# Kernel tuning notes

Hardware: AMD Instinct MI355X
Metric: run time of the kernel (lower is better)

The kernel has to match this reference:

```python
import jax, jax.numpy as jnp
import numpy as np

LN_EPS = 1e-6          # flax nn.LayerNorm default
ATTN_EPS = 1e-9        # numerical_stabilizer default


def ln_points(x, scale, bias):
    """flax LayerNorm(reduction_axes=-2): stats over points axis, affine over feature axis."""
    mu = jnp.mean(x, axis=-2, keepdims=True)
    var = jnp.mean(jnp.square(x), axis=-2, keepdims=True) - jnp.square(mu)
    return (x - mu) * jax.lax.rsqrt(var + LN_EPS) * scale + bias


def self_attention_layer(x, wq_i, bq_i, wk_i, bk_i, wv_i, bv_i, wo_i, bo_i, ls_i, lb_i):
    # 1x1 convs == pointwise linears
    q = x @ wq_i + bq_i                                  # [B,N,C]
    k = x @ wk_i + bk_i
    v = x @ wv_i + bv_i
    attn = jnp.einsum('bmc,bnc->bmn', q, k)              # [B,M,N]
    attn = jax.nn.softmax(attn, axis=-1)
    # extra offset-attention renorm: divide by column sums (axis=1)
    attn = attn / (ATTN_EPS + jnp.sum(attn, axis=1, keepdims=True))
    # einsum '...MN,...NC->...NC' reduces M: scales v by column sums
    col = jnp.sum(attn, axis=1)                          # [B,N]
    out = col[..., None] * v                             # [B,N,C]
    out = out @ wo_i + bo_i
    out = jax.nn.relu(ln_points(out, ls_i, lb_i))
    return out + x


def setup_inputs() -> dict:
    key = jax.random.key(0)
    ks = jax.random.split(key, 16)
    B, N, IN, C, F, L = 2, 4096, 3, 256, 1024, 4
    s_in = 1.0 / np.sqrt(IN)
    s_c = 1.0 / np.sqrt(C)
    s_f = 1.0 / np.sqrt(L * C)
    return {
        'inputs': jax.random.normal(ks[0], (B, N, IN), jnp.float32),
        'w0': jax.random.normal(ks[1], (IN, C), jnp.float32) * s_in,
        'b0': jnp.zeros((C,), jnp.float32),
        'ln0_s': jnp.ones((C,), jnp.float32),
        'ln0_b': jnp.zeros((C,), jnp.float32),
        'w1': jax.random.normal(ks[2], (C, C), jnp.float32) * s_c,
        'b1': jnp.zeros((C,), jnp.float32),
        'ln1_s': jnp.ones((C,), jnp.float32),
        'ln1_b': jnp.zeros((C,), jnp.float32),
        'wq': jax.random.normal(ks[3], (L, C, C), jnp.float32) * s_c,
        'bq': jnp.zeros((L, C), jnp.float32),
        'wk': jax.random.normal(ks[4], (L, C, C), jnp.float32) * s_c,
        'bk': jnp.zeros((L, C), jnp.float32),
        'wv': jax.random.normal(ks[5], (L, C, C), jnp.float32) * s_c,
        'bv': jnp.zeros((L, C), jnp.float32),
        'wo': jax.random.normal(ks[6], (L, C, C), jnp.float32) * s_c,
        'bo': jnp.zeros((L, C), jnp.float32),
        'attn_ln_s': jnp.ones((L, C), jnp.float32),
        'attn_ln_b': jnp.zeros((L, C), jnp.float32),
        'wf': jax.random.normal(ks[7], (L * C, F), jnp.float32) * s_f,
        'bf': jnp.zeros((F,), jnp.float32),
    }


def reference(inputs, w0, b0, ln0_s, ln0_b, w1, b1, ln1_s, ln1_b,
              wq, bq, wk, bk, wv, bv, wo, bo, attn_ln_s, attn_ln_b, wf, bf):
    # pre-conv stack
    out = ln_points(inputs @ w0 + b0, ln0_s, ln0_b)
    out = ln_points(out @ w1 + b1, ln1_s, ln1_b)
    # attention stack (4 structurally identical layers, concatenated)
    attn_outs = []
    for i in range(wq.shape[0]):
        out = self_attention_layer(out, wq[i], bq[i], wk[i], bk[i],
                                   wv[i], bv[i], wo[i], bo[i],
                                   attn_ln_s[i], attn_ln_b[i])
        attn_outs.append(out)
    out = jnp.concatenate(attn_outs, axis=-1)            # [B,N,4C]
    out = out @ wf + bf                                  # [B,N,F]
    return out
```

## Files before the change

### kernel.cpp

```cpp
#include <hip/hip_runtime.h>

#define BB 2
#define NN 4096
#define CC 256
#define FF 1024
#define NLAYER 4
#define RR (BB*NN)
#define SPL 16
#define QKLD (3*CC)
#define NEG_BIG (-1e30f)
#define LOG2E 1.44269504f

typedef _Float16 h16;
typedef __attribute__((ext_vector_type(8))) _Float16 half8;
typedef __attribute__((ext_vector_type(4))) float f32x4;
typedef __attribute__((ext_vector_type(16))) float f32x16;

#define WAITVM(n) asm volatile("s_waitcnt vmcnt(" #n ")" ::: "memory")

__device__ __forceinline__ void gload16(const h16* g, h16* l) {
    __builtin_amdgcn_global_load_lds((const __attribute__((address_space(1))) void*)g,
                                     (__attribute__((address_space(3))) void*)l, 16, 0, 0);
}

template<int ROWS>
__device__ __forceinline__ void stage_rows(const h16* __restrict__ src, int ld,
    int row0, int c0, h16* lds, int tid)
{
    int w = tid >> 6;
    #pragma unroll
    for (int t = 0; t < ROWS/32; ++t) {
        int slot = t*256 + tid;
        int row = slot >> 3;
        int pp  = slot & 7;
        int piece = pp ^ (row & 7);
        gload16(src + (size_t)(row0 + row)*ld + c0 + piece*8,
                lds + (t*256 + w*64)*8);
    }
}

__device__ __forceinline__ half8 frag_ld(const h16* lds, int row, int pl) {
    return *(const half8*)(lds + row*64 + ((pl ^ (row & 7))*8));
}

__global__ __launch_bounds__(256) void pct_wtrans(const float* __restrict__ W,
    h16* __restrict__ WT, int K, int N, int dstride, float scale)
{
    __shared__ h16 t[32][33];
    const float* Wl = W + (size_t)blockIdx.z*K*N;
    h16* WTl = WT + (size_t)blockIdx.z*dstride;
    int k0 = blockIdx.x*32, n0 = blockIdx.y*32;
    int tx = threadIdx.x & 31, ty = threadIdx.x >> 5;
    #pragma unroll
    for (int i = ty; i < 32; i += 8)
        t[i][tx] = (h16)(Wl[(size_t)(k0+i)*N + n0 + tx] * scale);
    __syncthreads();
    #pragma unroll
    for (int i = ty; i < 32; i += 8)
        WTl[(size_t)(n0+i)*K + k0 + tx] = t[tx][i];
}

__global__ __launch_bounds__(256) void pct_wtrans_qkv(const float* __restrict__ wq,
    const float* __restrict__ wk, const float* __restrict__ wv, h16* __restrict__ WT)
{
    __shared__ h16 t[32][33];
    int z = blockIdx.z;
    int which = z >> 2, layer = z & 3;
    const float* Wl = (which == 0 ? wq : which == 1 ? wk : wv) + (size_t)layer*CC*CC;
    h16* WTl = WT + (size_t)layer*QKLD*CC + (size_t)which*CC*CC;
    float scale = (which == 0) ? LOG2E : 1.0f;
    int k0 = blockIdx.x*32, n0 = blockIdx.y*32;
    int tx = threadIdx.x & 31, ty = threadIdx.x >> 5;
    #pragma unroll
    for (int i = ty; i < 32; i += 8)
        t[i][tx] = (h16)(Wl[(size_t)(k0+i)*CC + n0 + tx] * scale);
    __syncthreads();
    #pragma unroll
    for (int i = ty; i < 32; i += 8)
        WTl[(size_t)(n0+i)*CC + k0 + tx] = t[tx][i];
}

__global__ __launch_bounds__(256) void pct_bias3(const float* __restrict__ bq,
    const float* __restrict__ bk, const float* __restrict__ bv, float* __restrict__ o)
{
    int l = blockIdx.x, c = threadIdx.x;
    o[l*QKLD + c]        = bq[l*CC + c] * LOG2E;
    o[l*QKLD + CC + c]   = bk[l*CC + c];
    o[l*QKLD + 2*CC + c] = bv[l*CC + c];
}

__global__ __launch_bounds__(256) void pct_embed(const float* __restrict__ inp,
    const float* __restrict__ w0, const float* __restrict__ b0,
    h16* __restrict__ out, float* __restrict__ sums)
{
    int c = threadIdx.x;
    int r0 = blockIdx.x * 64;
    float wa = w0[c], wb = w0[CC+c], wcv = w0[2*CC+c], bb = b0[c];
    float s1 = 0.f, s2 = 0.f;
    #pragma unroll 4
    for (int i = 0; i < 64; ++i) {
        int r = r0 + i;
        float y = bb + inp[r*3+0]*wa + inp[r*3+1]*wb + inp[r*3+2]*wcv;
        h16 hy = (h16)y;
        out[(size_t)r*CC + c] = hy;
        float yf = (float)hy;
        s1 += yf; s2 += yf*yf;
    }
    int b = r0 >> 12;
    atomicAdd(&sums[((size_t)b*CC + c)*2 + 0], s1);
    atomicAdd(&sums[((size_t)b*CC + c)*2 + 1], s2);
}

__global__ __launch_bounds__(256) void pct_lnapply(const h16* __restrict__ x, int ldx,
    const float* __restrict__ sums, const float* __restrict__ scale, const float* __restrict__ bias,
    const h16* __restrict__ res, int ldr, h16* __restrict__ out, int ldo,
    int do_relu)
{
    int r = blockIdx.x*8 + (threadIdx.x >> 5);
    int cg = (threadIdx.x & 31) * 8;
    int b = r / NN;
    half8 xv = *(const half8*)(x + (size_t)r*ldx + cg);
    half8 rv;
    if (res) rv = *(const half8*)(res + (size_t)r*ldr + cg);
    half8 ov;
    #pragma unroll
    for (int j = 0; j < 8; ++j) {
        int c = cg + j;
        float s1 = sums[(b*CC + c)*2], s2 = sums[(b*CC + c)*2 + 1];
        float mu  = s1 * (1.f/NN);
        float var = s2 * (1.f/NN) - mu*mu;
        float rstd = rsqrtf(var + 1e-6f);
        float y = ((float)xv[j] - mu) * rstd * scale[c] + bias[c];
        if (do_relu) y = fmaxf(y, 0.f);
        if (res) y += (float)rv[j];
        ov[j] = (h16)y;
    }
    *(half8*)(out + (size_t)r*ldo + cg) = ov;
}

template<int BN, bool OUT_F32, bool CSTAT>
__global__ __launch_bounds__(256) void pct_gemm_f16(
    const h16* __restrict__ A, int lda,
    const h16* __restrict__ WT, const float* __restrict__ bias,
    void* __restrict__ outp, int ldo, int K, const float* __restrict__ rowS,
    float* __restrict__ csums)
{
    constexpr int BJ = BN/2;
    constexpr int NF = BJ/16;
    __shared__ __align__(16) h16 Asm[128*64];
    __shared__ __align__(16) h16 Bsm[BN*64];
    const int tid = threadIdx.x;
    const int lane = tid & 63, w = tid >> 6;
    const int ln = lane & 15, lq = lane >> 4;
    const int wr = w >> 1, wc = w & 1;
    const int m0 = blockIdx.x*128, n0 = blockIdx.y*BN;
    f32x4 acc[4][NF];
    #pragma unroll
    for (int i = 0; i < 4; ++i)
        #pragma unroll
        for (int j = 0; j < NF; ++j) acc[i][j] = (f32x4){0.f,0.f,0.f,0.f};
    for (int k0 = 0; k0 < K; k0 += 64) {
        stage_rows<128>(A, lda, m0, k0, Asm, tid);
        stage_rows<BN>(WT, K, n0, k0, Bsm, tid);
        __syncthreads();
        #pragma unroll
        for (int kk = 0; kk < 2; ++kk) {
            half8 af[4], bfr[NF];
            #pragma unroll
            for (int i = 0; i < 4; ++i) af[i] = frag_ld(Asm, wr*64 + i*16 + ln, kk*4 + lq);
            #pragma unroll
            for (int j = 0; j < NF; ++j) bfr[j] = frag_ld(Bsm, wc*BJ + j*16 + ln, kk*4 + lq);
            #pragma unroll
            for (int i = 0; i < 4; ++i)
                #pragma unroll
                for (int j = 0; j < NF; ++j)
                    acc[i][j] = __builtin_amdgcn_mfma_f32_16x16x32_f16(af[i], bfr[j], acc[i][j], 0, 0, 0);
        }
        __syncthreads();
    }
    float cs1[NF], cs2[NF];
    #pragma unroll
    for (int j = 0; j < NF; ++j) {
        int col = n0 + wc*BJ + j*16 + ln;
        float bv = bias[col];
        float s1 = 0.f, s2 = 0.f;
        #pragma unroll
        for (int i = 0; i < 4; ++i) {
            #pragma unroll
            for (int r = 0; r < 4; ++r) {
                int row = m0 + wr*64 + i*16 + lq*4 + r;
                float sc = 1.f;
                if (rowS) { float s = rowS[row]; sc = s / (1e-9f + s); }
                float v = acc[i][j][r] * sc + bv;
                if (OUT_F32) ((float*)outp)[(size_t)row*ldo + col] = v;
                else ((h16*)outp)[(size_t)row*ldo + col] = (h16)v;
                if (CSTAT) { s1 += v; s2 += v*v; }
            }
        }
        cs1[j] = s1; cs2[j] = s2;
    }
    if constexpr (CSTAT) {
        __shared__ float cred[2][2][BJ][2];
        #pragma unroll
        for (int j = 0; j < NF; ++j) {
            float s1 = cs1[j], s2 = cs2[j];
            s1 += __shfl_down(s1, 16); s1 += __shfl_down(s1, 32);
            s2 += __shfl_down(s2, 16); s2 += __shfl_down(s2, 32);
            if (lane < 16) {
                cred[wr][wc][j*16 + lane][0] = s1;
                cred[wr][wc][j*16 + lane][1] = s2;
            }
        }
        __syncthreads();
        if (tid < 2*BN) {
            int c = tid >> 1, st = tid & 1;
            int wcc = c >> 5, ci = c & 31;
            float v = cred[0][wcc][ci][st] + cred[1][wcc][ci][st];
            int b = m0 >> 12;
            atomicAdd(&csums[((size_t)b*CC + n0 + c)*2 + st], v);
        }
    }
}

__global__ __launch_bounds__(256) void attn_rowstats(const h16* __restrict__ QKV,
    float2* __restrict__ part)
{
    __shared__ __align__(16) h16 Ks[2][128*64];
    const int b = blockIdx.x, mt = blockIdx.y, sp = blockIdx.z;
    const int tid = threadIdx.x;
    const int lane = tid & 63, w = tid >> 6;
    const int ln2 = lane & 31, h = lane >> 5;
    const h16* qb = QKV + (size_t)b*NN*QKLD;
    const h16* kb = qb + CC;
    const int m0 = mt*128;
    const h16* qrow = qb + (size_t)(m0 + w*32 + ln2)*QKLD + h*8;
    half8 qreg[16];
    #pragma unroll
    for (int i = 0; i < 16; ++i) qreg[i] = *(const half8*)(qrow + i*16);

    const int nbeg = sp*(NN/SPL);
    constexpr int NT = (NN/SPL)/128;
    constexpr int NCH = NT*4;
    float rm = NEG_BIG, rs = 0.f;

    stage_rows<128>(kb, QKLD, nbeg, 0, Ks[0], tid);
    int id = 0;
    #pragma unroll
    for (int t = 0; t < NT; ++t) {
        f32x16 acc[4];
        #pragma unroll
        for (int j = 0; j < 4; ++j) acc[j] = (f32x16)(0.f);
        #pragma unroll
        for (int c = 0; c < 4; ++c, ++id) {
            if (id + 1 < NCH) {
                stage_rows<128>(kb, QKLD, nbeg + ((id+1) >> 2)*128, ((id+1) & 3)*64,
                                Ks[(id+1) & 1], tid);
                WAITVM(4);
            } else {
                WAITVM(0);
            }
            __builtin_amdgcn_s_barrier();
            const h16* buf = Ks[id & 1];
            __builtin_amdgcn_s_setprio(1);
            #pragma unroll
            for (int kk = 0; kk < 4; ++kk) {
                half8 bq = qreg[c*4 + kk];
                #pragma unroll
                for (int j = 0; j < 4; ++j) {
                    half8 af = frag_ld(buf, j*32 + ln2, kk*2 + h);
                    acc[j] = __builtin_amdgcn_mfma_f32_32x32x16_f16(af, bq, acc[j], 0, 0, 0);
                }
            }
            __builtin_amdgcn_s_setprio(0);
            __builtin_amdgcn_s_barrier();
        }
        float tm = NEG_BIG;
        #pragma unroll
        for (int j = 0; j < 4; ++j)
            #pragma unroll
            for (int g = 0; g < 16; g += 2)
                tm = fmaxf(tm, fmaxf(acc[j][g], acc[j][g+1]));
        if (tm > rm) { rs *= exp2f(rm - tm); rm = tm; }
        float s = 0.f;
        #pragma unroll
        for (int j = 0; j < 4; ++j)
            #pragma unroll
            for (int g = 0; g < 16; ++g)
                s += exp2f(acc[j][g] - rm);
        rs += s;
    }
    float mo = __shfl_xor(rm, 32, 64);
    float so = __shfl_xor(rs, 32, 64);
    float mn = fmaxf(rm, mo);
    float sm = rs*exp2f(rm - mn) + so*exp2f(mo - mn);
    if (lane < 32) {
        int m = m0 + w*32 + ln2;
        part[((size_t)b*NN + m)*SPL + sp] = make_float2(mn, sm);
    }
}

__global__ __launch_bounds__(256) void attn_colsums(const h16* __restrict__ QKV,
    const float2* __restrict__ part, float* __restrict__ S)
{
    __shared__ __align__(16) h16 Qs[2][128*64];
    __shared__ float2 rst_s[256];
    const int b = blockIdx.x, nt = blockIdx.y, sp = blockIdx.z;
    const int tid = threadIdx.x;
    const int lane = tid & 63, w = tid >> 6;
    const int ln2 = lane & 31, h = lane >> 5;
    const h16* qb = QKV + (size_t)b*NN*QKLD;
    const h16* kb = qb + CC;
    const int n0 = nt*128;
    const int mbeg = sp*(NN/SPL);

    {
        const float2* pp = part + ((size_t)b*NN + mbeg + tid)*SPL;
        float m = NEG_BIG;
        #pragma unroll
        for (int s = 0; s < SPL; ++s) m = fmaxf(m, pp[s].x);
        float sum = 0.f;
        #pragma unroll
        for (int s = 0; s < SPL; ++s) sum += pp[s].y * exp2f(pp[s].x - m);
        rst_s[tid] = make_float2(m, 1.0f / sum);
    }
    __syncthreads();

    const h16* krow = kb + (size_t)(n0 + w*32 + ln2)*QKLD + h*8;
    half8 kreg[16];
    #pragma unroll
    for (int i = 0; i < 16; ++i) kreg[i] = *(const half8*)(krow + i*16);

    constexpr int NT = (NN/SPL)/128;
    constexpr int NCH = NT*4;
    float cs = 0.f;

    stage_rows<128>(qb, QKLD, mbeg, 0, Qs[0], tid);
    int id = 0;
    #pragma unroll
    for (int t = 0; t < NT; ++t) {
        f32x16 acc[4];
        #pragma unroll
        for (int j = 0; j < 4; ++j) acc[j] = (f32x16)(0.f);
        #pragma unroll
        for (int c = 0; c < 4; ++c, ++id) {
            if (id + 1 < NCH) {
                stage_rows<128>(qb, QKLD, mbeg + ((id+1) >> 2)*128, ((id+1) & 3)*64,
                                Qs[(id+1) & 1], tid);
                WAITVM(4);
            } else {
                WAITVM(0);
            }
            __builtin_amdgcn_s_barrier();
            const h16* buf = Qs[id & 1];
            __builtin_amdgcn_s_setprio(1);
            #pragma unroll
            for (int kk = 0; kk < 4; ++kk) {
                half8 bk = kreg[c*4 + kk];
                #pragma unroll
                for (int j = 0; j < 4; ++j) {
                    half8 af = frag_ld(buf, j*32 + ln2, kk*2 + h);
                    acc[j] = __builtin_amdgcn_mfma_f32_32x32x16_f16(af, bk, acc[j], 0, 0, 0);
                }
            }
            __builtin_amdgcn_s_setprio(0);
            __builtin_amdgcn_s_barrier();
        }
        int mt0 = t*128;
        #pragma unroll
        for (int j = 0; j < 4; ++j) {
            #pragma unroll
            for (int g = 0; g < 16; ++g) {
                int mloc = mt0 + j*32 + (g & 3) + 8*(g >> 2) + 4*h;
                float2 st = rst_s[mloc];
                cs += exp2f(acc[j][g] - st.x) * st.y;
            }
        }
    }
    cs += __shfl_xor(cs, 32, 64);
    if (lane < 32) {
        int n = n0 + w*32 + ln2;
        atomicAdd(&S[(size_t)b*NN + n], cs);
    }
}

extern "C" void kernel_launch(void* const* d_in, const int* in_sizes, int n_in,
                              void* d_out, int out_size, void* d_ws, size_t ws_size,
                              hipStream_t stream)
{
    const float* inp  = (const float*)d_in[0];
    const float* w0   = (const float*)d_in[1];
    const float* b0   = (const float*)d_in[2];
    const float* ln0s = (const float*)d_in[3];
    const float* ln0b = (const float*)d_in[4];
    const float* w1   = (const float*)d_in[5];
    const float* b1   = (const float*)d_in[6];
    const float* ln1s = (const float*)d_in[7];
    const float* ln1b = (const float*)d_in[8];
    const float* wq   = (const float*)d_in[9];
    const float* bq   = (const float*)d_in[10];
    const float* wk   = (const float*)d_in[11];
    const float* bk   = (const float*)d_in[12];
    const float* wv   = (const float*)d_in[13];
    const float* bv   = (const float*)d_in[14];
    const float* wo   = (const float*)d_in[15];
    const float* bo   = (const float*)d_in[16];
    const float* alns = (const float*)d_in[17];
    const float* alnb = (const float*)d_in[18];
    const float* wf   = (const float*)d_in[19];
    const float* bfb  = (const float*)d_in[20];
    float* out = (float*)d_out;

    char* p = (char*)d_ws;
    auto alloc = [&](size_t bytes) { char* r = p; p += (bytes + 255) & ~255ULL; return r; };
    h16* t0    = (h16*)alloc((size_t)RR*CC*2);
    h16* t1    = (h16*)alloc((size_t)RR*CC*2);
    h16* t2    = (h16*)alloc((size_t)RR*CC*2);
    h16* x1    = (h16*)alloc((size_t)RR*CC*2);
    h16* qkv   = (h16*)alloc((size_t)RR*QKLD*2);
    h16* oh    = (h16*)alloc((size_t)RR*CC*2);
    h16* xcat  = (h16*)alloc((size_t)RR*FF*2);
    h16* w1T   = (h16*)alloc((size_t)CC*CC*2);
    h16* wqkvT = (h16*)alloc((size_t)NLAYER*QKLD*CC*2);
    h16* woT   = (h16*)alloc((size_t)NLAYER*CC*CC*2);
    h16* wfT   = (h16*)alloc((size_t)FF*FF*2);
    float* bqkv  = (float*)alloc((size_t)NLAYER*QKLD*4);
    float2* part  = (float2*)alloc((size_t)RR*SPL*8);
    float* Ssum  = (float*)alloc((size_t)NLAYER*RR*4);
    float* lns   = (float*)alloc((size_t)6*BB*CC*2*4);

    dim3 blk(256);

    hipMemsetAsync(Ssum, 0, (size_t)((char*)(lns + 6*BB*CC*2) - (char*)Ssum), stream);

    pct_wtrans<<<dim3(CC/32, CC/32, 1), blk, 0, stream>>>(w1, w1T, CC, CC, CC*CC, 1.f);
    pct_wtrans_qkv<<<dim3(CC/32, CC/32, 3*NLAYER), blk, 0, stream>>>(wq, wk, wv, wqkvT);
    pct_wtrans<<<dim3(CC/32, CC/32, NLAYER), blk, 0, stream>>>(wo, woT, CC, CC, CC*CC, 1.f);
    pct_wtrans<<<dim3(FF/32, FF/32, 1), blk, 0, stream>>>(wf, wfT, FF, FF, FF*FF, 1.f);
    pct_bias3<<<NLAYER, blk, 0, stream>>>(bq, bk, bv, bqkv);

    pct_embed<<<RR/64, blk, 0, stream>>>(inp, w0, b0, t0, lns + 0*BB*CC*2);
    pct_lnapply<<<RR/8, blk, 0, stream>>>(t0, CC, lns + 0*BB*CC*2, ln0s, ln0b, nullptr, 0, t1, CC, 0);
    pct_gemm_f16<64,false,true><<<dim3(RR/128, CC/64), blk, 0, stream>>>(
        t1, CC, w1T, b1, t2, CC, CC, nullptr, lns + 1*BB*CC*2);
    pct_lnapply<<<RR/8, blk, 0, stream>>>(t2, CC, lns + 1*BB*CC*2, ln1s, ln1b, nullptr, 0, x1, CC, 0);

    const h16* xin = x1; int ldx = CC;
    for (int i = 0; i < NLAYER; ++i) {
        pct_gemm_f16<64,false,false><<<dim3(RR/128, QKLD/64), blk, 0, stream>>>(
            xin, ldx, wqkvT + (size_t)i*QKLD*CC, bqkv + i*QKLD, qkv, QKLD, CC, nullptr, nullptr);

        attn_rowstats<<<dim3(BB, NN/128, SPL), blk, 0, stream>>>(qkv, part);
        attn_colsums<<<dim3(BB, NN/128, SPL), blk, 0, stream>>>(qkv, part, Ssum + (size_t)i*RR);

        pct_gemm_f16<64,false,true><<<dim3(RR/128, CC/64), blk, 0, stream>>>(
            qkv + 2*CC, QKLD, woT + (size_t)i*CC*CC, bo + i*CC, oh, CC, CC,
            Ssum + (size_t)i*RR, lns + (2+i)*BB*CC*2);

        pct_lnapply<<<RR/8, blk, 0, stream>>>(oh, CC, lns + (2+i)*BB*CC*2, alns + i*CC, alnb + i*CC,
                                              xin, ldx, xcat + i*CC, FF, 1);
        xin = xcat + i*CC; ldx = FF;
    }

    pct_gemm_f16<128,true,false><<<dim3(RR/128, FF/128), blk, 0, stream>>>(
        xcat, FF, wfT, bfb, out, FF, FF, nullptr, nullptr);
}
```

Measured before the change: 497.6 us.

## Interleave K/Q prefetch with MFMA steps and remap attention grid per XCD

The two attention kernels now issue the next tile's global-to-LDS loads one piece per kk step, after that step's fragments are read, so the copy is spread across the compute. The old code issued the whole stage up front and waited on a partial vmcnt. The wait is now a full vmcnt(0) at the top of each chunk, and the MFMA priority bump is narrowed to each group of four MFMAs. The grids are flattened to 1D and block ids are remapped so each XCD's blocks share one batch and neighbouring row tiles, which aims to improve L2 reuse of K and Q. Prefetch time now has less slack, and the full wait could expose load latency.

```diff
diff --git a/kernel.cpp b/kernel.cpp
--- a/kernel.cpp
+++ b/kernel.cpp
@@ -37,6 +37,18 @@
         gload16(src + (size_t)(row0 + row)*ld + c0 + piece*8,
                 lds + (t*256 + w*64)*8);
     }
+}
+
+__device__ __forceinline__ void stage_piece(const h16* __restrict__ src, int ld,
+    int row0, int c0, h16* lds, int tid, int t)
+{
+    int w = tid >> 6;
+    int slot = t*256 + tid;
+    int row = slot >> 3;
+    int pp  = slot & 7;
+    int piece = pp ^ (row & 7);
+    gload16(src + (size_t)(row0 + row)*ld + c0 + piece*8,
+            lds + (t*256 + w*64)*8);
 }
 
 __device__ __forceinline__ half8 frag_ld(const h16* lds, int row, int pl) {
@@ -226,7 +238,11 @@
     float2* __restrict__ part)
 {
     __shared__ __align__(16) h16 Ks[2][128*64];
-    const int b = blockIdx.x, mt = blockIdx.y, sp = blockIdx.z;
+    const int lid = blockIdx.x;
+    const int xcd = lid & 7;
+    const int b   = xcd >> 2;
+    const int r   = (lid >> 3)*4 + (xcd & 3);
+    const int mt  = r >> 4, sp = r & 15;
     const int tid = threadIdx.x;
     const int lane = tid & 63, w = tid >> 6;
     const int ln2 = lane & 31, h = lane >> 5;
@@ -252,26 +268,25 @@
         for (int j = 0; j < 4; ++j) acc[j] = (f32x16)(0.f);
         #pragma unroll
         for (int c = 0; c < 4; ++c, ++id) {
-            if (id + 1 < NCH) {
-                stage_rows<128>(kb, QKLD, nbeg + ((id+1) >> 2)*128, ((id+1) & 3)*64,
-                                Ks[(id+1) & 1], tid);
-                WAITVM(4);
-            } else {
-                WAITVM(0);
-            }
+            WAITVM(0);
             __builtin_amdgcn_s_barrier();
             const h16* buf = Ks[id & 1];
-            __builtin_amdgcn_s_setprio(1);
+            const bool pf = (id + 1 < NCH);
+            const int prow = pf ? nbeg + ((id+1) >> 2)*128 : 0;
+            const int pcol = pf ? ((id+1) & 3)*64 : 0;
             #pragma unroll
             for (int kk = 0; kk < 4; ++kk) {
+                half8 af[4];
+                #pragma unroll
+                for (int j = 0; j < 4; ++j) af[j] = frag_ld(buf, j*32 + ln2, kk*2 + h);
+                if (pf) stage_piece(kb, QKLD, prow, pcol, Ks[(id+1) & 1], tid, kk);
                 half8 bq = qreg[c*4 + kk];
+                __builtin_amdgcn_s_setprio(1);
                 #pragma unroll
-                for (int j = 0; j < 4; ++j) {
-                    half8 af = frag_ld(buf, j*32 + ln2, kk*2 + h);
-                    acc[j] = __builtin_amdgcn_mfma_f32_32x32x16_f16(af, bq, acc[j], 0, 0, 0);
-                }
+                for (int j = 0; j < 4; ++j)
+                    acc[j] = __builtin_amdgcn_mfma_f32_32x32x16_f16(af[j], bq, acc[j], 0, 0, 0);
+                __builtin_amdgcn_s_setprio(0);
             }
-            __builtin_amdgcn_s_setprio(0);
             __builtin_amdgcn_s_barrier();
         }
         float tm = NEG_BIG;
@@ -304,7 +319,11 @@
 {
     __shared__ __align__(16) h16 Qs[2][128*64];
     __shared__ float2 rst_s[256];
-    const int b = blockIdx.x, nt = blockIdx.y, sp = blockIdx.z;
+    const int lid = blockIdx.x;
+    const int xcd = lid & 7;
+    const int b   = xcd >> 2;
+    const int r   = (lid >> 3)*4 + (xcd & 3);
+    const int nt  = r >> 4, sp = r & 15;
     const int tid = threadIdx.x;
     const int lane = tid & 63, w = tid >> 6;
     const int ln2 = lane & 31, h = lane >> 5;
@@ -343,26 +362,25 @@
         for (int j = 0; j < 4; ++j) acc[j] = (f32x16)(0.f);
         #pragma unroll
         for (int c = 0; c < 4; ++c, ++id) {
-            if (id + 1 < NCH) {
-                stage_rows<128>(qb, QKLD, mbeg + ((id+1) >> 2)*128, ((id+1) & 3)*64,
-                                Qs[(id+1) & 1], tid);
-                WAITVM(4);
-            } else {
-                WAITVM(0);
-            }
+            WAITVM(0);
             __builtin_amdgcn_s_barrier();
             const h16* buf = Qs[id & 1];
-            __builtin_amdgcn_s_setprio(1);
+            const bool pf = (id + 1 < NCH);
+            const int prow = pf ? mbeg + ((id+1) >> 2)*128 : 0;
+            const int pcol = pf ? ((id+1) & 3)*64 : 0;
             #pragma unroll
             for (int kk = 0; kk < 4; ++kk) {
+                half8 af[4];
+                #pragma unroll
+                for (int j = 0; j < 4; ++j) af[j] = frag_ld(buf, j*32 + ln2, kk*2 + h);
+                if (pf) stage_piece(qb, QKLD, prow, pcol, Qs[(id+1) & 1], tid, kk);
                 half8 bk = kreg[c*4 + kk];
+                __builtin_amdgcn_s_setprio(1);
                 #pragma unroll
-                for (int j = 0; j < 4; ++j) {
-                    half8 af = frag_ld(buf, j*32 + ln2, kk*2 + h);
-                    acc[j] = __builtin_amdgcn_mfma_f32_32x32x16_f16(af, bk, acc[j], 0, 0, 0);
-                }
+                for (int j = 0; j < 4; ++j)
+                    acc[j] = __builtin_amdgcn_mfma_f32_32x32x16_f16(af[j], bk, acc[j], 0, 0, 0);
+                __builtin_amdgcn_s_setprio(0);
             }
-            __builtin_amdgcn_s_setprio(0);
             __builtin_amdgcn_s_barrier();
         }
         int mt0 = t*128;
@@ -449,8 +467,8 @@
         pct_gemm_f16<64,false,false><<<dim3(RR/128, QKLD/64), blk, 0, stream>>>(
             xin, ldx, wqkvT + (size_t)i*QKLD*CC, bqkv + i*QKLD, qkv, QKLD, CC, nullptr, nullptr);
 
-        attn_rowstats<<<dim3(BB, NN/128, SPL), blk, 0, stream>>>(qkv, part);
-        attn_colsums<<<dim3(BB, NN/128, SPL), blk, 0, stream>>>(qkv, part, Ssum + (size_t)i*RR);
+        attn_rowstats<<<dim3(BB*(NN/128)*SPL), blk, 0, stream>>>(qkv, part);
+        attn_colsums<<<dim3(BB*(NN/128)*SPL), blk, 0, stream>>>(qkv, part, Ssum + (size_t)i*RR);
 
         pct_gemm_f16<64,false,true><<<dim3(RR/128, CC/64), blk, 0, stream>>>(
             qkv + 2*CC, QKLD, woT + (size_t)i*CC*CC, bo + i*CC, oh, CC, CC,
```

Result: slower. 518.5 us (+4.2%).

## Use 2x2 warp tiling in attention row-stat and column-sum kernels

Applied to the files above, without the earlier changes.

Changes the warp decomposition in attn_rowstats and attn_colsums from each warp owning 32 register rows against all 128 LDS rows to a 2x2 layout. Each warp now owns 64 register rows against 64 LDS rows, which halves the LDS fragment loads per MFMA and reuses each LDS fragment for two MFMAs. Row-stat partials double since each row now gets two partial max/sum pairs, so the partial buffer and the colsum merge loop grow accordingly. Register pressure rises (two sets of Q/K registers) and launch_bounds now requests 2 blocks per SIMD-group, which may cause spills.

```diff
diff --git a/kernel.cpp b/kernel.cpp
--- a/kernel.cpp
+++ b/kernel.cpp
@@ -222,7 +222,7 @@
     }
 }
 
-__global__ __launch_bounds__(256) void attn_rowstats(const h16* __restrict__ QKV,
+__global__ __launch_bounds__(256, 2) void attn_rowstats(const h16* __restrict__ QKV,
     float2* __restrict__ part)
 {
     __shared__ __align__(16) h16 Ks[2][128*64];
@@ -230,26 +230,32 @@
     const int tid = threadIdx.x;
     const int lane = tid & 63, w = tid >> 6;
     const int ln2 = lane & 31, h = lane >> 5;
+    const int wn = w & 1, wm = w >> 1;
     const h16* qb = QKV + (size_t)b*NN*QKLD;
     const h16* kb = qb + CC;
     const int m0 = mt*128;
-    const h16* qrow = qb + (size_t)(m0 + w*32 + ln2)*QKLD + h*8;
-    half8 qreg[16];
-    #pragma unroll
-    for (int i = 0; i < 16; ++i) qreg[i] = *(const half8*)(qrow + i*16);
+    half8 qreg[2][16];
+    #pragma unroll
+    for (int mh = 0; mh < 2; ++mh) {
+        const h16* qrow = qb + (size_t)(m0 + wm*64 + mh*32 + ln2)*QKLD + h*8;
+        #pragma unroll
+        for (int i = 0; i < 16; ++i) qreg[mh][i] = *(const half8*)(qrow + i*16);
+    }
 
     const int nbeg = sp*(NN/SPL);
     constexpr int NT = (NN/SPL)/128;
     constexpr int NCH = NT*4;
-    float rm = NEG_BIG, rs = 0.f;
+    float rm[2] = {NEG_BIG, NEG_BIG}, rs[2] = {0.f, 0.f};
 
     stage_rows<128>(kb, QKLD, nbeg, 0, Ks[0], tid);
     int id = 0;
     #pragma unroll
     for (int t = 0; t < NT; ++t) {
-        f32x16 acc[4];
-        #pragma unroll
-        for (int j = 0; j < 4; ++j) acc[j] = (f32x16)(0.f);
+        f32x16 acc[2][2];
+        #pragma unroll
+        for (int j = 0; j < 2; ++j)
+            #pragma unroll
+            for (int mh = 0; mh < 2; ++mh) acc[j][mh] = (f32x16)(0.f);
         #pragma unroll
         for (int c = 0; c < 4; ++c, ++id) {
             if (id + 1 < NCH) {
@@ -264,42 +270,52 @@
             __builtin_amdgcn_s_setprio(1);
             #pragma unroll
             for (int kk = 0; kk < 4; ++kk) {
-                half8 bq = qreg[c*4 + kk];
-                #pragma unroll
-                for (int j = 0; j < 4; ++j) {
-                    half8 af = frag_ld(buf, j*32 + ln2, kk*2 + h);
-                    acc[j] = __builtin_amdgcn_mfma_f32_32x32x16_f16(af, bq, acc[j], 0, 0, 0);
-                }
+                half8 af[2];
+                #pragma unroll
+                for (int j = 0; j < 2; ++j)
+                    af[j] = frag_ld(buf, wn*64 + j*32 + ln2, kk*2 + h);
+                #pragma unroll
+                for (int j = 0; j < 2; ++j)
+                    #pragma unroll
+                    for (int mh = 0; mh < 2; ++mh)
+                        acc[j][mh] = __builtin_amdgcn_mfma_f32_32x32x16_f16(
+                            af[j], qreg[mh][c*4 + kk], acc[j][mh], 0, 0, 0);
             }
             __builtin_amdgcn_s_setprio(0);
             __builtin_amdgcn_s_barrier();
         }
-        float tm = NEG_BIG;
-        #pragma unroll
-        for (int j = 0; j < 4; ++j)
-            #pragma unroll
-            for (int g = 0; g < 16; g += 2)
-                tm = fmaxf(tm, fmaxf(acc[j][g], acc[j][g+1]));
-        if (tm > rm) { rs *= exp2f(rm - tm); rm = tm; }
-        float s = 0.f;
-        #pragma unroll
-        for (int j = 0; j < 4; ++j)
-            #pragma unroll
-            for (int g = 0; g < 16; ++g)
-                s += exp2f(acc[j][g] - rm);
-        rs += s;
-    }
-    float mo = __shfl_xor(rm, 32, 64);
-    float so = __shfl_xor(rs, 32, 64);
-    float mn = fmaxf(rm, mo);
-    float sm = rs*exp2f(rm - mn) + so*exp2f(mo - mn);
-    if (lane < 32) {
-        int m = m0 + w*32 + ln2;
-        part[((size_t)b*NN + m)*SPL + sp] = make_float2(mn, sm);
-    }
-}
-
-__global__ __launch_bounds__(256) void attn_colsums(const h16* __restrict__ QKV,
+        #pragma unroll
+        for (int mh = 0; mh < 2; ++mh) {
+            float tm = NEG_BIG;
+            #pragma unroll
+            for (int j = 0; j < 2; ++j)
+                #pragma unroll
+                for (int g = 0; g < 16; g += 2)
+                    tm = fmaxf(tm, fmaxf(acc[j][mh][g], acc[j][mh][g+1]));
+            if (tm > rm[mh]) { rs[mh] *= exp2f(rm[mh] - tm); rm[mh] = tm; }
+            float s = 0.f;
+            #pragma unroll
+            for (int j = 0; j < 2; ++j)
+                #pragma unroll
+                for (int g = 0; g < 16; ++g)
+                    s += exp2f(acc[j][mh][g] - rm[mh]);
+            rs[mh] += s;
+        }
+    }
+    #pragma unroll
+    for (int mh = 0; mh < 2; ++mh) {
+        float mo = __shfl_xor(rm[mh], 32, 64);
+        float so = __shfl_xor(rs[mh], 32, 64);
+        float mn = fmaxf(rm[mh], mo);
+        float sm = rs[mh]*exp2f(rm[mh] - mn) + so*exp2f(mo - mn);
+        if (lane < 32) {
+            int m = m0 + wm*64 + mh*32 + ln2;
+            part[(((size_t)b*NN + m)*SPL + sp)*2 + wn] = make_float2(mn, sm);
+        }
+    }
+}
+
+__global__ __launch_bounds__(256, 2) void attn_colsums(const h16* __restrict__ QKV,
     const float2* __restrict__ part, float* __restrict__ S)
 {
     __shared__ __align__(16) h16 Qs[2][128*64];
@@ -308,39 +324,45 @@
     const int tid = threadIdx.x;
     const int lane = tid & 63, w = tid >> 6;
     const int ln2 = lane & 31, h = lane >> 5;
+    const int ws = w & 1, wn2 = w >> 1;
     const h16* qb = QKV + (size_t)b*NN*QKLD;
     const h16* kb = qb + CC;
     const int n0 = nt*128;
     const int mbeg = sp*(NN/SPL);
 
     {
-        const float2* pp = part + ((size_t)b*NN + mbeg + tid)*SPL;
+        const float2* pp = part + ((size_t)b*NN + mbeg + tid)*SPL*2;
         float m = NEG_BIG;
         #pragma unroll
-        for (int s = 0; s < SPL; ++s) m = fmaxf(m, pp[s].x);
+        for (int s = 0; s < SPL*2; ++s) m = fmaxf(m, pp[s].x);
         float sum = 0.f;
         #pragma unroll
-        for (int s = 0; s < SPL; ++s) sum += pp[s].y * exp2f(pp[s].x - m);
+        for (int s = 0; s < SPL*2; ++s) sum += pp[s].y * exp2f(pp[s].x - m);
         rst_s[tid] = make_float2(m, 1.0f / sum);
     }
     __syncthreads();
 
-    const h16* krow = kb + (size_t)(n0 + w*32 + ln2)*QKLD + h*8;
-    half8 kreg[16];
-    #pragma unroll
-    for (int i = 0; i < 16; ++i) kreg[i] = *(const half8*)(krow + i*16);
+    half8 kreg[2][16];
+    #pragma unroll
+    for (int nh = 0; nh < 2; ++nh) {
+        const h16* krow = kb + (size_t)(n0 + wn2*64 + nh*32 + ln2)*QKLD + h*8;
+        #pragma unroll
+        for (int i = 0; i < 16; ++i) kreg[nh][i] = *(const half8*)(krow + i*16);
+    }
 
     constexpr int NT = (NN/SPL)/128;
     constexpr int NCH = NT*4;
-    float cs = 0.f;
+    float cs[2] = {0.f, 0.f};
 
     stage_rows<128>(qb, QKLD, mbeg, 0, Qs[0], tid);
     int id = 0;
     #pragma unroll
     for (int t = 0; t < NT; ++t) {
-        f32x16 acc[4];
-        #pragma unroll
-        for (int j = 0; j < 4; ++j) acc[j] = (f32x16)(0.f);
+        f32x16 acc[2][2];
+        #pragma unroll
+        for (int js = 0; js < 2; ++js)
+            #pragma unroll
+            for (int nh = 0; nh < 2; ++nh) acc[js][nh] = (f32x16)(0.f);
         #pragma unroll
         for (int c = 0; c < 4; ++c, ++id) {
             if (id + 1 < NCH) {
@@ -355,31 +377,41 @@
             __builtin_amdgcn_s_setprio(1);
             #pragma unroll
             for (int kk = 0; kk < 4; ++kk) {
-                half8 bk = kreg[c*4 + kk];
-                #pragma unroll
-                for (int j = 0; j < 4; ++j) {
-                    half8 af = frag_ld(buf, j*32 + ln2, kk*2 + h);
-                    acc[j] = __builtin_amdgcn_mfma_f32_32x32x16_f16(af, bk, acc[j], 0, 0, 0);
-                }
+                half8 af[2];
+                #pragma unroll
+                for (int js = 0; js < 2; ++js)
+                    af[js] = frag_ld(buf, ws*64 + js*32 + ln2, kk*2 + h);
+                #pragma unroll
+                for (int js = 0; js < 2; ++js)
+                    #pragma unroll
+                    for (int nh = 0; nh < 2; ++nh)
+                        acc[js][nh] = __builtin_amdgcn_mfma_f32_32x32x16_f16(
+                            af[js], kreg[nh][c*4 + kk], acc[js][nh], 0, 0, 0);
             }
             __builtin_amdgcn_s_setprio(0);
             __builtin_amdgcn_s_barrier();
         }
         int mt0 = t*128;
         #pragma unroll
-        for (int j = 0; j < 4; ++j) {
-            #pragma unroll
-            for (int g = 0; g < 16; ++g) {
-                int mloc = mt0 + j*32 + (g & 3) + 8*(g >> 2) + 4*h;
-                float2 st = rst_s[mloc];
-                cs += exp2f(acc[j][g] - st.x) * st.y;
-            }
-        }
-    }
-    cs += __shfl_xor(cs, 32, 64);
-    if (lane < 32) {
-        int n = n0 + w*32 + ln2;
-        atomicAdd(&S[(size_t)b*NN + n], cs);
+        for (int js = 0; js < 2; ++js) {
+            #pragma unroll
+            for (int nh = 0; nh < 2; ++nh) {
+                #pragma unroll
+                for (int g = 0; g < 16; ++g) {
+                    int mloc = mt0 + ws*64 + js*32 + (g & 3) + 8*(g >> 2) + 4*h;
+                    float2 st = rst_s[mloc];
+                    cs[nh] += exp2f(acc[js][nh][g] - st.x) * st.y;
+                }
+            }
+        }
+    }
+    #pragma unroll
+    for (int nh = 0; nh < 2; ++nh) {
+        cs[nh] += __shfl_xor(cs[nh], 32, 64);
+        if (lane < 32) {
+            int n = n0 + wn2*64 + nh*32 + ln2;
+            atomicAdd(&S[(size_t)b*NN + n], cs[nh]);
+        }
     }
 }
 
@@ -424,7 +456,7 @@
     h16* woT   = (h16*)alloc((size_t)NLAYER*CC*CC*2);
     h16* wfT   = (h16*)alloc((size_t)FF*FF*2);
     float* bqkv  = (float*)alloc((size_t)NLAYER*QKLD*4);
-    float2* part  = (float2*)alloc((size_t)RR*SPL*8);
+    float2* part  = (float2*)alloc((size_t)RR*SPL*2*8);
     float* Ssum  = (float*)alloc((size_t)NLAYER*RR*4);
     float* lns   = (float*)alloc((size_t)6*BB*CC*2*4);
 
```

Result: slower. 597.5 us (+20.1%).
